# Kernel optimization log

Hardware: AMD Instinct MI355X
Metric: run time of the kernel (lower is better)

Reference implementation:

```python
import jax, jax.numpy as jnp
import numpy as np

H = 128        # num_hidden
V = 32000      # vocab_size
CD = 256       # channel_dim
T = 21         # max_seq_len (hardcoded in forward_rl)
NS = 5         # multiple_sample default
SOS, EOS = 1, 2


def setup_inputs() -> dict:
    key = jax.random.key(0)
    ks = jax.random.split(key, 12)
    s = 0.08  # param scale ~ 1/sqrt(H)
    f32 = jnp.float32
    return {
        "input_features": jax.random.normal(ks[0], (1024, CD), f32),
        "embed": (jax.random.normal(ks[1], (V, H), f32) * s),
        "W_fc": jax.random.normal(ks[2], (2 * H, CD), f32) * s,
        "b_fc": jnp.zeros((2 * H,), f32),
        "W_ih": jax.random.normal(ks[3], (4 * H, H), f32) * s,
        "b_ih": jnp.zeros((4 * H,), f32),
        "W_hh": jax.random.normal(ks[4], (4 * H, H), f32) * s,
        "b_hh": jnp.zeros((4 * H,), f32),
        "W1": jax.random.normal(ks[5], (H, H), f32) * s,
        "b1": jnp.zeros((H,), f32),
        "W2": jax.random.normal(ks[6], (V, H), f32) * s,
        "b2": jnp.zeros((V,), f32),
    }


def _decode(input_features, embed, W_fc, b_fc, W_ih, b_ih, W_hh, b_hh, W1, b1, W2, b2):
    # sample_n_times: expand each row NS times along batch
    x = jnp.repeat(input_features, NS, axis=0)           # [B, CD], B = 1024*NS
    B = x.shape[0]
    # init_hidden: from_channel_emb -> split into (h, c)
    hc = x @ W_fc.T + b_fc                               # [B, 2H]
    h0, c0 = hc[:, :H], hc[:, H:]

    it0 = jnp.full((B,), SOS, jnp.int32)
    unf0 = jnp.ones((B,), bool)

    def step(carry, _):
        h, c, it, unfinished = carry
        xt = embed[it]                                   # [B, H]
        gates = xt @ W_ih.T + b_ih + h @ W_hh.T + b_hh   # [B, 4H]
        i, f, g, o = jnp.split(gates, 4, axis=1)         # torch LSTMCell gate order
        c_new = jax.nn.sigmoid(f) * c + jax.nn.sigmoid(i) * jnp.tanh(g)
        h_new = jax.nn.sigmoid(o) * jnp.tanh(c_new)
        # classifier: Linear -> Dropout(eval: identity) -> Linear
        logits = (h_new @ W1.T + b1) @ W2.T + b2         # [B, V]
        logprobs = jax.nn.log_softmax(logits, axis=-1)
        # deterministic sampling surrogate (sample_max path): argmax
        it_new = jnp.argmax(logprobs, axis=1).astype(jnp.int32)
        sample_lp = jnp.take_along_axis(logprobs, it_new[:, None], axis=1)[:, 0]
        mask = unfinished.astype(logprobs.dtype)
        it_new = jnp.where(unfinished, it_new, 0)
        unf_new = unfinished & (it_new != EOS)
        return (h_new, c_new, it_new, unf_new), (it_new, sample_lp, mask)

    _, (seq, lps, masks) = jax.lax.scan(step, (h0, c0, it0, unf0), None, length=T)
    # scan stacks along time: [T, B] -> [B, T]
    return seq.T, lps.T, masks.T


def reference(input_features, embed, W_fc, b_fc, W_ih, b_ih, W_hh, b_hh, W1, b1, W2, b2):
    return _decode(input_features, embed, W_fc, b_fc, W_ih, b_ih, W_hh, b_hh, W1, b1, W2, b2)
```

## Files before the change

### kernel.cpp

```cpp
#include <hip/hip_runtime.h>
#include <math.h>
#include <limits.h>

#define H 128
#define V 32000
#define CD 256
#define T_STEPS 21
#define NS 5
#define SOS 1
#define EOS 2
#define B 1024
#define BFULL 5120
#define NCHUNK 250

typedef _Float16 f16;
typedef f16   half8   __attribute__((ext_vector_type(8)));
typedef float floatx4 __attribute__((ext_vector_type(4)));
typedef unsigned short ushort8v __attribute__((ext_vector_type(8)));

#define AS1 __attribute__((address_space(1)))
#define AS3 __attribute__((address_space(3)))

__device__ __forceinline__ float bf2f(unsigned short u) {
    return __uint_as_float(((unsigned)u) << 16);
}

__device__ __forceinline__ float sig32(float x) {
    float t = (float)exp(-(double)x);
    float r = __fadd_rn(1.0f, t);
    return __fdiv_rn(1.0f, r);
}
__device__ __forceinline__ float tanh32(float x) { return (float)tanh((double)x); }

__device__ __forceinline__ double w2dot(const float* __restrict__ pr,
                                        const void* __restrict__ W2_raw,
                                        int v, bool isf) {
    double acc = 0.0;
    if (isf) {
        const float* wv = (const float*)W2_raw + (long)v * H;
        #pragma unroll 8
        for (int k4 = 0; k4 < H / 4; ++k4) {
            float4 wq = *(const float4*)(wv + k4 * 4);
            float4 pq = *(const float4*)(pr + k4 * 4);
            acc += (double)pq.x * (double)wq.x;
            acc += (double)pq.y * (double)wq.y;
            acc += (double)pq.z * (double)wq.z;
            acc += (double)pq.w * (double)wq.w;
        }
    } else {
        const unsigned short* wv = (const unsigned short*)W2_raw + (long)v * H;
        #pragma unroll 8
        for (int k4 = 0; k4 < H / 4; ++k4) {
            ushort4 u = *(const ushort4*)(wv + k4 * 4);
            float4 pq = *(const float4*)(pr + k4 * 4);
            acc += (double)pq.x * (double)bf2f(u.x);
            acc += (double)pq.y * (double)bf2f(u.y);
            acc += (double)pq.z * (double)bf2f(u.z);
            acc += (double)pq.w * (double)bf2f(u.w);
        }
    }
    return acc;
}

__global__ void k_detect(const unsigned short* __restrict__ e, int* __restrict__ flag) {
    int i = threadIdx.x;
    unsigned short u = e[2 * i];
    int ex = (u >> 7) & 0xFF;
    bool wild = ((u & 0x7FFF) != 0) && (ex < 0x60 || ex > 0x8F);
    unsigned long long m = __ballot(wild);
    if (i == 0) *flag = (m != 0ull) ? 1 : 0;
}

struct TCArgs {
    const void* src[12];
    float*      dst[12];
    int         n[12];
};
__global__ __launch_bounds__(256) void k_transcode_all(TCArgs tc, const int* __restrict__ flag) {
    int which = blockIdx.y;
    float* d = tc.dst[which];
    if (d == nullptr) return;
    int i = blockIdx.x * 256 + threadIdx.x;
    if (i >= tc.n[which]) return;
    if (*flag) d[i] = ((const float*)tc.src[which])[i];
    else       d[i] = bf2f(((const unsigned short*)tc.src[which])[i]);
}

__global__ __launch_bounds__(256) void k_wtr(
    const float* __restrict__ Wih, const float* __restrict__ Whh,
    const float* __restrict__ W1, float* __restrict__ wihT,
    float* __restrict__ whhT, float* __restrict__ w1T) {
    int e = blockIdx.x * 256 + threadIdx.x;
    if (e < 512 * 128) {
        int col = e >> 7, k = e & 127;
        wihT[(k >> 1) * 1024 + col * 2 + (k & 1)] = Wih[e];
    } else if (e < 2 * 512 * 128) {
        int i = e - 512 * 128;
        int col = i >> 7, k = i & 127;
        whhT[(k >> 1) * 1024 + col * 2 + (k & 1)] = Whh[i];
    } else if (e < 2 * 512 * 128 + 128 * 128) {
        int i = e - 2 * 512 * 128;
        int col = i >> 7, k = i & 127;
        w1T[(k >> 1) * 256 + col * 2 + (k & 1)] = W1[i];
    }
}

__global__ __launch_bounds__(256) void k_wsplit(
    const void* __restrict__ W2_raw, unsigned short* __restrict__ wh,
    unsigned short* __restrict__ wl, float* __restrict__ wn,
    const int* __restrict__ flag) {
    int t = blockIdx.x * 256 + threadIdx.x;
    const bool isf = (*flag != 0);
    int vrow = t >> 4;
    int kkg  = t & 15;
    float v[8];
    if (isf) {
        float4 f0 = ((const float4*)W2_raw)[2 * t];
        float4 f1 = ((const float4*)W2_raw)[2 * t + 1];
        v[0] = f0.x; v[1] = f0.y; v[2] = f0.z; v[3] = f0.w;
        v[4] = f1.x; v[5] = f1.y; v[6] = f1.z; v[7] = f1.w;
    } else {
        ushort8v u = ((const ushort8v*)W2_raw)[t];
        #pragma unroll
        for (int i = 0; i < 8; ++i) v[i] = bf2f(u[i]);
    }
    float s = 0.f;
    half8 hv, lv;
    #pragma unroll
    for (int i = 0; i < 8; ++i) {
        s += v[i] * v[i];
        float ws = v[i] * 256.0f;
        f16 hh = (f16)ws;
        hv[i] = hh;
        lv[i] = (f16)(ws - (float)hh);
    }
    int cb = vrow >> 7, rloc = vrow & 127;
    long dst = (long)cb * 16384 + kkg * 1024 + rloc * 8;
    *(half8*)((f16*)wh + dst) = hv;
    *(half8*)((f16*)wl + dst) = lv;
    #pragma unroll
    for (int off = 1; off < 16; off <<= 1) s += __shfl_xor(s, off, 64);
    if (kkg == 0) wn[vrow] = sqrtf(s);
}

__global__ __launch_bounds__(256) void k_prep(
    const float* __restrict__ wn, float* __restrict__ wmax,
    int* __restrict__ it, int* __restrict__ unf) {
    int tid = threadIdx.x;
    if (blockIdx.x < 4) {
        int i = blockIdx.x * 256 + tid;
        it[i] = SOS; unf[i] = 1;
        return;
    }
    __shared__ float red[4];
    float m = 0.f;
    for (int i = tid; i < V; i += 256) m = fmaxf(m, wn[i]);
    #pragma unroll
    for (int off = 1; off < 64; off <<= 1) m = fmaxf(m, __shfl_xor(m, off, 64));
    if ((tid & 63) == 0) red[tid >> 6] = m;
    __syncthreads();
    if (tid == 0) *wmax = fmaxf(fmaxf(red[0], red[1]), fmaxf(red[2], red[3]));
}

__global__ __launch_bounds__(256) void k_init_hc(
    const float* __restrict__ xf, const float* __restrict__ Wfc,
    const float* __restrict__ bfc, float* __restrict__ h, float* __restrict__ c) {
    __shared__ float xl[CD];
    int r = blockIdx.x;
    int j = threadIdx.x;
    xl[j] = xf[(long)r * CD + j];
    __syncthreads();
    const float4* w4 = (const float4*)(Wfc + (long)j * CD);
    double acc = 0.0;
    for (int k4 = 0; k4 < CD / 4; ++k4) {
        float4 w = w4[k4];
        int k = k4 * 4;
        acc += (double)xl[k]     * (double)w.x;
        acc += (double)xl[k + 1] * (double)w.y;
        acc += (double)xl[k + 2] * (double)w.z;
        acc += (double)xl[k + 3] * (double)w.w;
    }
    float hc = __fadd_rn((float)acc, bfc[j]);
    if (j < H) h[(long)r * H + j] = hc;
    else       c[(long)r * H + (j - H)] = hc;
}

__global__ __launch_bounds__(512) void k_gf(
    const float* __restrict__ cmT, const float* __restrict__ csT,
    const unsigned long long* __restrict__ maskbuf,
    const void* __restrict__ W2_raw,
    const float* __restrict__ b2, const float* __restrict__ wmax,
    const void* __restrict__ embed_raw, float* __restrict__ h, float* __restrict__ c,
    const float* __restrict__ wihT, const float* __restrict__ whhT,
    const float* __restrict__ bih, const float* __restrict__ bhh,
    const float* __restrict__ w1T, const float* __restrict__ b1,
    float* __restrict__ p32, unsigned short* __restrict__ ph,
    unsigned short* __restrict__ pl, float* __restrict__ pnorm,
    int* __restrict__ it, int* __restrict__ unf, float* __restrict__ out,
    int t, const int* __restrict__ flag) {
    __shared__ float As[4][256];
    __shared__ float gsh[4][512];
    __shared__ float hl[4][132];
    __shared__ float redp[8];
    const bool isf = (*flag != 0);
    int tid = threadIdx.x;
    int rb = blockIdx.x * 4;
    int lane = tid & 63, wid = tid >> 6;

    if (t > 0 && wid < 4) {
        int r = rb + wid;
        const float* pr = p32 + (long)r * H;
        float wmx = *wmax;
        float eps = 6.0e-5f * pnorm[r] * wmx + 3e-5f;

        float marr[4];
        float AM = -__builtin_inff();
        #pragma unroll
        for (int i = 0; i < 4; ++i) {
            int cc = lane + 64 * i;
            marr[i] = (cc < NCHUNK) ? cmT[(long)cc * B + r] : -__builtin_inff();
            AM = fmaxf(AM, marr[i]);
        }
        #pragma unroll
        for (int off = 1; off < 64; off <<= 1) AM = fmaxf(AM, __shfl_xor(AM, off, 64));
        double S = 0.0;
        #pragma unroll
        for (int i = 0; i < 4; ++i) {
            int cc = lane + 64 * i;
            if (cc < NCHUNK) S += (double)csT[(long)cc * B + r];
        }
        #pragma unroll
        for (int off = 1; off < 64; off <<= 1) S += __shfl_xor(S, off, 64);

        float M = -__builtin_inff();
        #pragma unroll 1
        for (int i = 0; i < 4; ++i) {
            unsigned long long mask = __ballot(marr[i] >= AM - eps);
            while (mask) {
                int bsl = __ffsll(mask) - 1;
                mask &= mask - 1;
                int cc = i * 64 + bsl;
                const unsigned long long* mk2 = maskbuf + ((long)cc * B + r) * 2;
                #pragma unroll 1
                for (int q = 0; q < 2; ++q) {
                    if ((mk2[q] >> lane) & 1ull) {
                        int v = cc * 128 + q * 64 + lane;
                        double acc = w2dot(pr, W2_raw, v, isf);
                        float l = __fadd_rn((float)acc, b2[v]);
                        M = fmaxf(M, l);
                    }
                }
            }
        }
        #pragma unroll
        for (int off = 1; off < 64; off <<= 1) M = fmaxf(M, __shfl_xor(M, off, 64));

        float L = (float)(log(S) - (double)M);
        float negL = __fsub_rn(0.0f, L);

        int best = INT_MAX;
        #pragma unroll 1
        for (int i = 0; i < 4 && best == INT_MAX; ++i) {
            unsigned long long mask = __ballot(marr[i] >= AM - eps);
            while (mask && best == INT_MAX) {
                int bsl = __ffsll(mask) - 1;
                mask &= mask - 1;
                int cc = i * 64 + bsl;
                const unsigned long long* mk2 = maskbuf + ((long)cc * B + r) * 2;
                int hit = INT_MAX;
                #pragma unroll 1
                for (int q = 0; q < 2; ++q) {
                    if ((mk2[q] >> lane) & 1ull) {
                        int v = cc * 128 + q * 64 + lane;
                        double acc = w2dot(pr, W2_raw, v, isf);
                        float l  = __fadd_rn((float)acc, b2[v]);
                        float lp = __fsub_rn(__fsub_rn(l, M), L);
                        if (lp == negL && v < hit) hit = v;
                    }
                }
                #pragma unroll
                for (int off = 1; off < 64; off <<= 1) {
                    int oh = __shfl_xor(hit, off, 64);
                    hit = (oh < hit) ? oh : hit;
                }
                if (hit != INT_MAX) best = hit;
            }
        }
        int bi = (best == INT_MAX) ? 0 : best;

        int unfr = unf[r];
        float lp = negL;
        int itn = unfr ? bi : 0;
        int unfn = (unfr && itn != EOS) ? 1 : 0;
        if (lane == 0) { it[r] = itn; unf[r] = unfn; }
        if (lane < NS) {
            long ro = (long)r * NS + lane;
            int tm1 = t - 1;
            out[ro * T_STEPS + tm1] = (float)itn;
            out[(long)BFULL * T_STEPS + ro * T_STEPS + tm1] = lp;
            out[2L * BFULL * T_STEPS + ro * T_STEPS + tm1] = unfr ? 1.0f : 0.0f;
        }
    }
    __syncthreads();

    {
        int r = tid >> 7, kq = (tid & 127) * 2;
        long row = rb + r;
        int tok = it[row];
        float v0, v1;
        if (kq < H) {
            if (isf) {
                float2 f = *(const float2*)((const float*)embed_raw + (long)tok * H + kq);
                v0 = f.x; v1 = f.y;
            } else {
                ushort2 u = *(const ushort2*)((const unsigned short*)embed_raw + (long)tok * H + kq);
                v0 = bf2f(u.x); v1 = bf2f(u.y);
            }
        } else {
            float2 f = *(const float2*)(h + row * H + (kq - H));
            v0 = f.x; v1 = f.y;
        }
        As[r][kq] = v0; As[r][kq + 1] = v1;
    }
    __syncthreads();

    {
        int cg = tid;
        double acc[4] = {};
        const float2* wi2 = (const float2*)wihT + cg;
        #pragma unroll 8
        for (int kp = 0; kp < 64; ++kp) {
            float2 w = wi2[kp * 512];
            #pragma unroll
            for (int r = 0; r < 4; ++r) {
                float2 a2 = *(const float2*)(&As[r][kp * 2]);
                double s0 = acc[r];
                s0 += (double)a2.x * (double)w.x;
                s0 += (double)a2.y * (double)w.y;
                acc[r] = s0;
            }
        }
        float t1[4];
        float bi = bih[cg];
        #pragma unroll
        for (int r = 0; r < 4; ++r) {
            t1[r] = __fadd_rn((float)acc[r], bi);
            acc[r] = 0.0;
        }
        const float2* wh2 = (const float2*)whhT + cg;
        #pragma unroll 8
        for (int kp = 0; kp < 64; ++kp) {
            float2 w = wh2[kp * 512];
            #pragma unroll
            for (int r = 0; r < 4; ++r) {
                float2 a2 = *(const float2*)(&As[r][128 + kp * 2]);
                double s0 = acc[r];
                s0 += (double)a2.x * (double)w.x;
                s0 += (double)a2.y * (double)w.y;
                acc[r] = s0;
            }
        }
        float bh = bhh[cg];
        #pragma unroll
        for (int r = 0; r < 4; ++r)
            gsh[r][cg] = __fadd_rn(__fadd_rn(t1[r], (float)acc[r]), bh);
    }
    __syncthreads();

    {
        int lr = tid >> 7, j = tid & 127;
        long row = rb + lr;
        float gi = gsh[lr][j], gf = gsh[lr][j + 128], gg = gsh[lr][j + 256], go = gsh[lr][j + 384];
        float cv = c[row * 128 + j];
        float si = sig32(gi);
        float sf = sig32(gf);
        float so = sig32(go);
        float tg = tanh32(gg);
        float cn = __fadd_rn(__fmul_rn(sf, cv), __fmul_rn(si, tg));
        float hn = __fmul_rn(so, tanh32(cn));
        c[row * 128 + j] = cn;
        h[row * 128 + j] = hn;
        hl[lr][j] = hn;
    }
    __syncthreads();

    {
        int j = tid & 127;
        int rr = tid >> 7;
        const float2* w12 = (const float2*)w1T + j;
        double acc = 0.0;
        #pragma unroll 8
        for (int kp = 0; kp < 64; ++kp) {
            float2 w = w12[kp * 128];
            float2 a2 = *(const float2*)(&hl[rr][kp * 2]);
            acc += (double)a2.x * (double)w.x;
            acc += (double)a2.y * (double)w.y;
        }
        long row = rb + rr;
        float pv = __fadd_rn((float)acc, b1[j]);
        p32[row * H + j] = pv;
        float ps = pv * 256.0f;
        f16 hh = (f16)ps;
        f16 ll = (f16)(ps - (float)hh);
        ((f16*)ph)[row * H + j] = hh;
        ((f16*)pl)[row * H + j] = ll;
        float sq = pv * pv;
        #pragma unroll
        for (int off = 1; off < 64; off <<= 1) sq += __shfl_xor(sq, off, 64);
        if (lane == 0) redp[wid] = sq;
    }
    __syncthreads();
    if (tid < 4) pnorm[rb + tid] = sqrtf(redp[2 * tid] + redp[2 * tid + 1]);
}

__global__ __launch_bounds__(256, 2) void k_vscan_mfma(
    const unsigned short* __restrict__ ph_, const unsigned short* __restrict__ pl_,
    const unsigned short* __restrict__ whf_, const unsigned short* __restrict__ wlf_,
    const float* __restrict__ b2, const float* __restrict__ pnorm,
    const float* __restrict__ wmax,
    float* __restrict__ cmT, float* __restrict__ csT,
    unsigned long long* __restrict__ maskbuf) {
    __shared__ f16 Bsh[16384];
    __shared__ f16 Bsl[16384];
    const f16* ph  = (const f16*)ph_;
    const f16* pl  = (const f16*)pl_;
    int tid  = threadIdx.x;
    int lane = tid & 63, wid = tid >> 6;
    int tx = lane & 15, kg = lane >> 4;

    int bid = blockIdx.x;
    int xcd = bid & 7, rb = (bid >> 3) & 3, hi = bid >> 5;
    int cb = hi * 8 + xcd;
    if (cb >= NCHUNK) return;
    int rbw = rb * 256 + wid * 64;
    int vb  = cb * 128;

    {
        const f16* sh = (const f16*)whf_ + (long)cb * 16384;
        const f16* sl = (const f16*)wlf_ + (long)cb * 16384;
        #pragma unroll
        for (int i = 0; i < 8; ++i) {
            int g = tid + 256 * i;
            __builtin_amdgcn_global_load_lds(
                (const AS1 void*)(const void*)(sh + (long)g * 8),
                (AS3 void*)(void*)(Bsh + g * 8), 16, 0, 0);
            __builtin_amdgcn_global_load_lds(
                (const AS1 void*)(const void*)(sl + (long)g * 8),
                (AS3 void*)(void*)(Bsl + g * 8), 16, 0, 0);
        }
    }
    __syncthreads();

    floatx4 acc[4][8];
    #pragma unroll
    for (int m = 0; m < 4; ++m)
        #pragma unroll
        for (int n = 0; n < 8; ++n)
            acc[m][n] = (floatx4){0.f, 0.f, 0.f, 0.f};

    int aoffs[4];
    #pragma unroll
    for (int m = 0; m < 4; ++m) aoffs[m] = (rbw + m * 16 + tx) * H + kg * 8;

    #pragma unroll
    for (int kk = 0; kk < 4; ++kk) {
        half8 Ah[4], Al[4];
        #pragma unroll
        for (int m = 0; m < 4; ++m) {
            Ah[m] = *(const half8*)(ph + aoffs[m] + kk * 32);
            Al[m] = *(const half8*)(pl + aoffs[m] + kk * 32);
        }
        int bbase = (kk * 4 + kg) * 1024 + tx * 8;
        #pragma unroll
        for (int n = 0; n < 8; ++n) {
            half8 Bh = *(const half8*)(Bsh + bbase + n * 128);
            half8 Bl = *(const half8*)(Bsl + bbase + n * 128);
            #pragma unroll
            for (int m = 0; m < 4; ++m)
                acc[m][n] = __builtin_amdgcn_mfma_f32_16x16x32_f16(Ah[m], Bh, acc[m][n], 0, 0, 0);
            #pragma unroll
            for (int m = 0; m < 4; ++m)
                acc[m][n] = __builtin_amdgcn_mfma_f32_16x16x32_f16(Ah[m], Bl, acc[m][n], 0, 0, 0);
            #pragma unroll
            for (int m = 0; m < 4; ++m)
                acc[m][n] = __builtin_amdgcn_mfma_f32_16x16x32_f16(Al[m], Bh, acc[m][n], 0, 0, 0);
        }
    }

    const float S2 = 1.0f / 65536.0f;
    const float wmx = *wmax;
    float bb[8];
    #pragma unroll
    for (int n = 0; n < 8; ++n) bb[n] = b2[vb + n * 16 + tx];
    #pragma unroll
    for (int m = 0; m < 4; ++m) {
        #pragma unroll
        for (int r = 0; r < 4; ++r) {
            float l[8];
            float mxr = -__builtin_inff();
            float sr = 0.f;
            #pragma unroll
            for (int n = 0; n < 8; ++n) {
                l[n] = acc[m][n][r] * S2 + bb[n];
                mxr = fmaxf(mxr, l[n]);
                sr += __expf(l[n]);
            }
            #pragma unroll
            for (int off = 1; off < 16; off <<= 1) {
                mxr = fmaxf(mxr, __shfl_xor(mxr, off, 64));
                sr += __shfl_xor(sr, off, 64);
            }
            int row = rbw + m * 16 + kg * 4 + r;
            float thr = mxr - (6.0e-5f * pnorm[row] * wmx + 3.0e-5f);
            unsigned long long w0 = 0, w1 = 0;
            #pragma unroll
            for (int n = 0; n < 8; ++n) {
                unsigned long long bal = __ballot(l[n] >= thr);
                unsigned long long piece = (bal >> (kg * 16)) & 0xFFFFull;
                if (n < 4) w0 |= piece << (n * 16);
                else       w1 |= piece << ((n - 4) * 16);
            }
            if (tx == 0) {
                cmT[(long)cb * B + row] = mxr;
                csT[(long)cb * B + row] = sr;
                maskbuf[((long)cb * B + row) * 2]     = w0;
                maskbuf[((long)cb * B + row) * 2 + 1] = w1;
            }
        }
    }
}

__global__ __launch_bounds__(256) void k_final(
    const float* __restrict__ cmT, const float* __restrict__ csT,
    const unsigned long long* __restrict__ maskbuf,
    const float* __restrict__ p32, const void* __restrict__ W2_raw,
    const float* __restrict__ b2, const float* __restrict__ wmax,
    const float* __restrict__ pnorm,
    int* __restrict__ it, int* __restrict__ unf,
    float* __restrict__ out, int t, const int* __restrict__ flag) {
    const bool isf = (*flag != 0);
    int r = blockIdx.x * 4 + (threadIdx.x >> 6);
    int lane = threadIdx.x & 63;
    const float* pr = p32 + (long)r * H;
    float wmx = *wmax;
    float eps = 6.0e-5f * pnorm[r] * wmx + 3e-5f;

    float marr[4];
    float AM = -__builtin_inff();
    #pragma unroll
    for (int i = 0; i < 4; ++i) {
        int cc = lane + 64 * i;
        marr[i] = (cc < NCHUNK) ? cmT[(long)cc * B + r] : -__builtin_inff();
        AM = fmaxf(AM, marr[i]);
    }
    #pragma unroll
    for (int off = 1; off < 64; off <<= 1) AM = fmaxf(AM, __shfl_xor(AM, off, 64));
    double S = 0.0;
    #pragma unroll
    for (int i = 0; i < 4; ++i) {
        int cc = lane + 64 * i;
        if (cc < NCHUNK) S += (double)csT[(long)cc * B + r];
    }
    #pragma unroll
    for (int off = 1; off < 64; off <<= 1) S += __shfl_xor(S, off, 64);

    float M = -__builtin_inff();
    #pragma unroll 1
    for (int i = 0; i < 4; ++i) {
        unsigned long long mask = __ballot(marr[i] >= AM - eps);
        while (mask) {
            int b = __ffsll(mask) - 1;
            mask &= mask - 1;
            int cc = i * 64 + b;
            const unsigned long long* mk2 = maskbuf + ((long)cc * B + r) * 2;
            #pragma unroll 1
            for (int q = 0; q < 2; ++q) {
                if ((mk2[q] >> lane) & 1ull) {
                    int v = cc * 128 + q * 64 + lane;
                    double acc = w2dot(pr, W2_raw, v, isf);
                    float l = __fadd_rn((float)acc, b2[v]);
                    M = fmaxf(M, l);
                }
            }
        }
    }
    #pragma unroll
    for (int off = 1; off < 64; off <<= 1) M = fmaxf(M, __shfl_xor(M, off, 64));

    float L = (float)(log(S) - (double)M);
    float negL = __fsub_rn(0.0f, L);

    int best = INT_MAX;
    #pragma unroll 1
    for (int i = 0; i < 4 && best == INT_MAX; ++i) {
        unsigned long long mask = __ballot(marr[i] >= AM - eps);
        while (mask && best == INT_MAX) {
            int b = __ffsll(mask) - 1;
            mask &= mask - 1;
            int cc = i * 64 + b;
            const unsigned long long* mk2 = maskbuf + ((long)cc * B + r) * 2;
            int hit = INT_MAX;
            #pragma unroll 1
            for (int q = 0; q < 2; ++q) {
                if ((mk2[q] >> lane) & 1ull) {
                    int v = cc * 128 + q * 64 + lane;
                    double acc = w2dot(pr, W2_raw, v, isf);
                    float l  = __fadd_rn((float)acc, b2[v]);
                    float lp = __fsub_rn(__fsub_rn(l, M), L);
                    if (lp == negL && v < hit) hit = v;
                }
            }
            #pragma unroll
            for (int off = 1; off < 64; off <<= 1) {
                int oh = __shfl_xor(hit, off, 64);
                hit = (oh < hit) ? oh : hit;
            }
            if (hit != INT_MAX) best = hit;
        }
    }
    int bi = (best == INT_MAX) ? 0 : best;

    int unfr = unf[r];
    float lp = negL;
    int itn = unfr ? bi : 0;
    int unfn = (unfr && itn != EOS) ? 1 : 0;
    if (lane == 0) { it[r] = itn; unf[r] = unfn; }
    if (lane < NS) {
        long ro = (long)r * NS + lane;
        out[ro * T_STEPS + t] = (float)itn;
        out[(long)BFULL * T_STEPS + ro * T_STEPS + t] = lp;
        out[2L * BFULL * T_STEPS + ro * T_STEPS + t] = unfr ? 1.0f : 0.0f;
    }
}

extern "C" void kernel_launch(void* const* d_in, const int* in_sizes, int n_in,
                              void* d_out, int out_size, void* d_ws, size_t ws_size,
                              hipStream_t stream) {
    float* out = (float*)d_out;

    char* w = (char*)d_ws;
    float* fin[12];
    for (int i = 0; i < 12; ++i) {
        if (i == 1 || i == 10) { fin[i] = nullptr; continue; }
        fin[i] = (float*)w;
        size_t bytes = ((size_t)in_sizes[i] * 4 + 15) & ~(size_t)15;
        w += bytes;
    }
    float*  h     = (float*) w; w += (size_t)B * H * 4;
    float*  c     = (float*) w; w += (size_t)B * H * 4;
    float*  p32   = (float*) w; w += (size_t)B * H * 4;
    float*  cm    = (float*) w; w += (size_t)B * NCHUNK * 4;
    float*  cs    = (float*) w; w += (size_t)B * NCHUNK * 4;
    float*  wn    = (float*) w; w += (size_t)V * 4;
    float*  wmax  = (float*) w; w += 16;
    float*  pnorm = (float*) w; w += (size_t)B * 4;
    int*    it    = (int*)   w; w += (size_t)B * 4;
    int*    unf   = (int*)   w; w += (size_t)B * 4;
    int*    flag  = (int*)   w; w += 16;
    float*  wihT  = (float*) w; w += (size_t)512 * 128 * 4;
    float*  whhT  = (float*) w; w += (size_t)512 * 128 * 4;
    float*  w1T   = (float*) w; w += (size_t)128 * 128 * 4;
    unsigned long long* maskbuf = (unsigned long long*)w; w += (size_t)NCHUNK * B * 16;
    unsigned short* ph = (unsigned short*)w; w += (size_t)B * H * 2;
    unsigned short* pl = (unsigned short*)w; w += (size_t)B * H * 2;
    unsigned short* wh = (unsigned short*)w; w += (size_t)V * H * 2;
    unsigned short* wl = (unsigned short*)w; w += (size_t)V * H * 2;

    k_detect<<<1, 64, 0, stream>>>((const unsigned short*)d_in[1], flag);

    TCArgs tc;
    int maxn = 0;
    for (int i = 0; i < 12; ++i) {
        tc.src[i] = d_in[i];
        tc.dst[i] = fin[i];
        tc.n[i]   = in_sizes[i];
        if (fin[i] && in_sizes[i] > maxn) maxn = in_sizes[i];
    }
    k_transcode_all<<<dim3((maxn + 255) / 256, 12), 256, 0, stream>>>(tc, flag);

    k_wsplit<<<(V * H / 8 + 255) / 256, 256, 0, stream>>>(d_in[10], wh, wl, wn, flag);
    k_wtr<<<(2 * 512 * 128 + 128 * 128 + 255) / 256, 256, 0, stream>>>(
        fin[4], fin[6], fin[8], wihT, whhT, w1T);
    k_prep<<<5, 256, 0, stream>>>(wn, wmax, it, unf);

    const float* xf  = fin[0];
    const float* Wfc = fin[2];
    const float* bfc = fin[3];
    const float* bih = fin[5];
    const float* bhh = fin[7];
    const float* b1  = fin[9];
    const float* b2  = fin[11];

    k_init_hc<<<B, 256, 0, stream>>>(xf, Wfc, bfc, h, c);

    for (int t = 0; t < T_STEPS; ++t) {
        k_gf<<<B / 4, 512, 0, stream>>>(cm, cs, maskbuf, d_in[10], b2, wmax,
                                        d_in[1], h, c, wihT, whhT, bih, bhh,
                                        w1T, b1, p32, ph, pl, pnorm, it, unf, out, t, flag);
        k_vscan_mfma<<<1024, 256, 0, stream>>>(ph, pl, wh, wl, b2, pnorm, wmax, cm, cs, maskbuf);
    }
    k_final<<<B / 4, 256, 0, stream>>>(cm, cs, maskbuf, p32, d_in[10], b2, wmax, pnorm,
                                       it, unf, out, T_STEPS - 1, flag);
}
```

Baseline: 1.776 ms.

## Halve rows per gate block, cache candidate logits, byte-wise mask writes

k_gf now handles 2 rows per block instead of 4, launching twice as many blocks. It stages the per-chunk max and sum arrays in shared memory with coalesced float2 loads. It also keeps up to two candidate logits per lane from the max pass, so the argmax pass does not recompute the W2 dot products unless a lane has more than two candidates. k_vscan_mfma now writes the candidate mask as one byte per thread instead of ballot-packed 64-bit words, with a matching remapped bit test on the reader side. The risks are fewer rows sharing each weight load in the gate GEMV and scattered byte stores.

```diff
diff --git a/kernel.cpp b/kernel.cpp
--- a/kernel.cpp
+++ b/kernel.cpp
@@ -60,6 +60,12 @@
         }
     }
     return acc;
+}
+
+__device__ __forceinline__ bool mask_test(unsigned long long m0, unsigned long long m1, int c) {
+    int bidx = ((c & 15) << 3) + (c >> 4);
+    unsigned long long word = (bidx < 64) ? m0 : m1;
+    return (word >> (bidx & 63)) & 1ull;
 }
 
 __global__ void k_detect(const unsigned short* __restrict__ e, int* __restrict__ flag) {
@@ -198,16 +204,24 @@
     unsigned short* __restrict__ pl, float* __restrict__ pnorm,
     int* __restrict__ it, int* __restrict__ unf, float* __restrict__ out,
     int t, const int* __restrict__ flag) {
-    __shared__ float As[4][256];
-    __shared__ float gsh[4][512];
-    __shared__ float hl[4][132];
-    __shared__ float redp[8];
+    __shared__ float As[2][256];
+    __shared__ float gsh[2][512];
+    __shared__ float hl[2][132];
+    __shared__ float2 cmsh[256];
+    __shared__ float2 cssh[256];
+    __shared__ float redp[4];
     const bool isf = (*flag != 0);
     int tid = threadIdx.x;
-    int rb = blockIdx.x * 4;
+    int rb = blockIdx.x * 2;
     int lane = tid & 63, wid = tid >> 6;
 
-    if (t > 0 && wid < 4) {
+    if (t > 0 && tid < NCHUNK) {
+        cmsh[tid] = *(const float2*)(cmT + (long)tid * B + rb);
+        cssh[tid] = *(const float2*)(csT + (long)tid * B + rb);
+    }
+    __syncthreads();
+
+    if (t > 0 && wid < 2) {
         int r = rb + wid;
         const float* pr = p32 + (long)r * H;
         float wmx = *wmax;
@@ -218,7 +232,10 @@
         #pragma unroll
         for (int i = 0; i < 4; ++i) {
             int cc = lane + 64 * i;
-            marr[i] = (cc < NCHUNK) ? cmT[(long)cc * B + r] : -__builtin_inff();
+            if (cc < NCHUNK) {
+                float2 cv = cmsh[cc];
+                marr[i] = wid ? cv.y : cv.x;
+            } else marr[i] = -__builtin_inff();
             AM = fmaxf(AM, marr[i]);
         }
         #pragma unroll
@@ -227,12 +244,18 @@
         #pragma unroll
         for (int i = 0; i < 4; ++i) {
             int cc = lane + 64 * i;
-            if (cc < NCHUNK) S += (double)csT[(long)cc * B + r];
+            if (cc < NCHUNK) {
+                float2 sv = cssh[cc];
+                S += (double)(wid ? sv.y : sv.x);
+            }
         }
         #pragma unroll
         for (int off = 1; off < 64; off <<= 1) S += __shfl_xor(S, off, 64);
 
         float M = -__builtin_inff();
+        float l0f = 0.f, l1f = 0.f;
+        int v0i = 0, v1i = 0, nc = 0;
+        bool spill = false;
         #pragma unroll 1
         for (int i = 0; i < 4; ++i) {
             unsigned long long mask = __ballot(marr[i] >= AM - eps);
@@ -241,13 +264,18 @@
                 mask &= mask - 1;
                 int cc = i * 64 + bsl;
                 const unsigned long long* mk2 = maskbuf + ((long)cc * B + r) * 2;
+                unsigned long long m0 = mk2[0], m1 = mk2[1];
                 #pragma unroll 1
                 for (int q = 0; q < 2; ++q) {
-                    if ((mk2[q] >> lane) & 1ull) {
-                        int v = cc * 128 + q * 64 + lane;
+                    int cidx = q * 64 + lane;
+                    if (mask_test(m0, m1, cidx)) {
+                        int v = cc * 128 + cidx;
                         double acc = w2dot(pr, W2_raw, v, isf);
                         float l = __fadd_rn((float)acc, b2[v]);
                         M = fmaxf(M, l);
+                        if (nc == 0)      { l0f = l; v0i = v; nc = 1; }
+                        else if (nc == 1) { l1f = l; v1i = v; nc = 2; }
+                        else spill = true;
                     }
                 }
             }
@@ -259,31 +287,51 @@
         float negL = __fsub_rn(0.0f, L);
 
         int best = INT_MAX;
-        #pragma unroll 1
-        for (int i = 0; i < 4 && best == INT_MAX; ++i) {
-            unsigned long long mask = __ballot(marr[i] >= AM - eps);
-            while (mask && best == INT_MAX) {
-                int bsl = __ffsll(mask) - 1;
-                mask &= mask - 1;
-                int cc = i * 64 + bsl;
-                const unsigned long long* mk2 = maskbuf + ((long)cc * B + r) * 2;
-                int hit = INT_MAX;
-                #pragma unroll 1
-                for (int q = 0; q < 2; ++q) {
-                    if ((mk2[q] >> lane) & 1ull) {
-                        int v = cc * 128 + q * 64 + lane;
-                        double acc = w2dot(pr, W2_raw, v, isf);
-                        float l  = __fadd_rn((float)acc, b2[v]);
-                        float lp = __fsub_rn(__fsub_rn(l, M), L);
-                        if (lp == negL && v < hit) hit = v;
+        if (__ballot(spill) == 0ull) {
+            int hit = INT_MAX;
+            if (nc >= 1) {
+                float lp = __fsub_rn(__fsub_rn(l0f, M), L);
+                if (lp == negL) hit = v0i;
+            }
+            if (nc >= 2) {
+                float lp = __fsub_rn(__fsub_rn(l1f, M), L);
+                if (lp == negL && v1i < hit) hit = v1i;
+            }
+            #pragma unroll
+            for (int off = 1; off < 64; off <<= 1) {
+                int oh = __shfl_xor(hit, off, 64);
+                hit = (oh < hit) ? oh : hit;
+            }
+            best = hit;
+        } else {
+            #pragma unroll 1
+            for (int i = 0; i < 4 && best == INT_MAX; ++i) {
+                unsigned long long mask = __ballot(marr[i] >= AM - eps);
+                while (mask && best == INT_MAX) {
+                    int bsl = __ffsll(mask) - 1;
+                    mask &= mask - 1;
+                    int cc = i * 64 + bsl;
+                    const unsigned long long* mk2 = maskbuf + ((long)cc * B + r) * 2;
+                    unsigned long long m0 = mk2[0], m1 = mk2[1];
+                    int hit = INT_MAX;
+                    #pragma unroll 1
+                    for (int q = 0; q < 2; ++q) {
+                        int cidx = q * 64 + lane;
+                        if (mask_test(m0, m1, cidx)) {
+                            int v = cc * 128 + cidx;
+                            double acc = w2dot(pr, W2_raw, v, isf);
+                            float l  = __fadd_rn((float)acc, b2[v]);
+                            float lp = __fsub_rn(__fsub_rn(l, M), L);
+                            if (lp == negL && v < hit) hit = v;
+                        }
                     }
+                    #pragma unroll
+                    for (int off = 1; off < 64; off <<= 1) {
+                        int oh = __shfl_xor(hit, off, 64);
+                        hit = (oh < hit) ? oh : hit;
+                    }
+                    if (hit != INT_MAX) best = hit;
                 }
-                #pragma unroll
-                for (int off = 1; off < 64; off <<= 1) {
-                    int oh = __shfl_xor(hit, off, 64);
-                    hit = (oh < hit) ? oh : hit;
-                }
-                if (hit != INT_MAX) best = hit;
             }
         }
         int bi = (best == INT_MAX) ? 0 : best;
@@ -304,35 +352,29 @@
     __syncthreads();
 
     {
-        int r = tid >> 7, kq = (tid & 127) * 2;
+        int r = tid >> 8, kq = tid & 255;
         long row = rb + r;
         int tok = it[row];
-        float v0, v1;
+        float v0;
         if (kq < H) {
-            if (isf) {
-                float2 f = *(const float2*)((const float*)embed_raw + (long)tok * H + kq);
-                v0 = f.x; v1 = f.y;
-            } else {
-                ushort2 u = *(const ushort2*)((const unsigned short*)embed_raw + (long)tok * H + kq);
-                v0 = bf2f(u.x); v1 = bf2f(u.y);
-            }
+            if (isf) v0 = ((const float*)embed_raw)[(long)tok * H + kq];
+            else     v0 = bf2f(((const unsigned short*)embed_raw)[(long)tok * H + kq]);
         } else {
-            float2 f = *(const float2*)(h + row * H + (kq - H));
-            v0 = f.x; v1 = f.y;
-        }
-        As[r][kq] = v0; As[r][kq + 1] = v1;
+            v0 = h[row * H + (kq - H)];
+        }
+        As[r][kq] = v0;
     }
     __syncthreads();
 
     {
         int cg = tid;
-        double acc[4] = {};
+        double acc[2] = {};
         const float2* wi2 = (const float2*)wihT + cg;
         #pragma unroll 8
         for (int kp = 0; kp < 64; ++kp) {
             float2 w = wi2[kp * 512];
             #pragma unroll
-            for (int r = 0; r < 4; ++r) {
+            for (int r = 0; r < 2; ++r) {
                 float2 a2 = *(const float2*)(&As[r][kp * 2]);
                 double s0 = acc[r];
                 s0 += (double)a2.x * (double)w.x;
@@ -340,10 +382,10 @@
                 acc[r] = s0;
             }
         }
-        float t1[4];
+        float t1[2];
         float bi = bih[cg];
         #pragma unroll
-        for (int r = 0; r < 4; ++r) {
+        for (int r = 0; r < 2; ++r) {
             t1[r] = __fadd_rn((float)acc[r], bi);
             acc[r] = 0.0;
         }
@@ -352,7 +394,7 @@
         for (int kp = 0; kp < 64; ++kp) {
             float2 w = wh2[kp * 512];
             #pragma unroll
-            for (int r = 0; r < 4; ++r) {
+            for (int r = 0; r < 2; ++r) {
                 float2 a2 = *(const float2*)(&As[r][128 + kp * 2]);
                 double s0 = acc[r];
                 s0 += (double)a2.x * (double)w.x;
@@ -362,12 +404,12 @@
         }
         float bh = bhh[cg];
         #pragma unroll
-        for (int r = 0; r < 4; ++r)
+        for (int r = 0; r < 2; ++r)
             gsh[r][cg] = __fadd_rn(__fadd_rn(t1[r], (float)acc[r]), bh);
     }
     __syncthreads();
 
-    {
+    if (tid < 256) {
         int lr = tid >> 7, j = tid & 127;
         long row = rb + lr;
         float gi = gsh[lr][j], gf = gsh[lr][j + 128], gg = gsh[lr][j + 256], go = gsh[lr][j + 384];
@@ -384,7 +426,7 @@
     }
     __syncthreads();
 
-    {
+    if (tid < 256) {
         int j = tid & 127;
         int rr = tid >> 7;
         const float2* w12 = (const float2*)w1T + j;
@@ -410,7 +452,7 @@
         if (lane == 0) redp[wid] = sq;
     }
     __syncthreads();
-    if (tid < 4) pnorm[rb + tid] = sqrtf(redp[2 * tid] + redp[2 * tid + 1]);
+    if (tid < 2) pnorm[rb + tid] = sqrtf(redp[2 * tid] + redp[2 * tid + 1]);
 }
 
 __global__ __launch_bounds__(256, 2) void k_vscan_mfma(
@@ -512,19 +554,14 @@
             }
             int row = rbw + m * 16 + kg * 4 + r;
             float thr = mxr - (6.0e-5f * pnorm[row] * wmx + 3.0e-5f);
-            unsigned long long w0 = 0, w1 = 0;
-            #pragma unroll
-            for (int n = 0; n < 8; ++n) {
-                unsigned long long bal = __ballot(l[n] >= thr);
-                unsigned long long piece = (bal >> (kg * 16)) & 0xFFFFull;
-                if (n < 4) w0 |= piece << (n * 16);
-                else       w1 |= piece << ((n - 4) * 16);
-            }
+            unsigned mb = 0;
+            #pragma unroll
+            for (int n = 0; n < 8; ++n)
+                if (l[n] >= thr) mb |= (1u << n);
+            ((unsigned char*)maskbuf)[((long)cb * B + row) * 16 + tx] = (unsigned char)mb;
             if (tx == 0) {
                 cmT[(long)cb * B + row] = mxr;
                 csT[(long)cb * B + row] = sr;
-                maskbuf[((long)cb * B + row) * 2]     = w0;
-                maskbuf[((long)cb * B + row) * 2 + 1] = w1;
             }
         }
     }
@@ -573,10 +610,12 @@
             mask &= mask - 1;
             int cc = i * 64 + b;
             const unsigned long long* mk2 = maskbuf + ((long)cc * B + r) * 2;
+            unsigned long long m0 = mk2[0], m1 = mk2[1];
             #pragma unroll 1
             for (int q = 0; q < 2; ++q) {
-                if ((mk2[q] >> lane) & 1ull) {
-                    int v = cc * 128 + q * 64 + lane;
+                int cidx = q * 64 + lane;
+                if (mask_test(m0, m1, cidx)) {
+                    int v = cc * 128 + cidx;
                     double acc = w2dot(pr, W2_raw, v, isf);
                     float l = __fadd_rn((float)acc, b2[v]);
                     M = fmaxf(M, l);
@@ -599,11 +638,13 @@
             mask &= mask - 1;
             int cc = i * 64 + b;
             const unsigned long long* mk2 = maskbuf + ((long)cc * B + r) * 2;
+            unsigned long long m0 = mk2[0], m1 = mk2[1];
             int hit = INT_MAX;
             #pragma unroll 1
             for (int q = 0; q < 2; ++q) {
-                if ((mk2[q] >> lane) & 1ull) {
-                    int v = cc * 128 + q * 64 + lane;
+                int cidx = q * 64 + lane;
+                if (mask_test(m0, m1, cidx)) {
+                    int v = cc * 128 + cidx;
                     double acc = w2dot(pr, W2_raw, v, isf);
                     float l  = __fadd_rn((float)acc, b2[v]);
                     float lp = __fsub_rn(__fsub_rn(l, M), L);
@@ -694,7 +735,7 @@
     k_init_hc<<<B, 256, 0, stream>>>(xf, Wfc, bfc, h, c);
 
     for (int t = 0; t < T_STEPS; ++t) {
-        k_gf<<<B / 4, 512, 0, stream>>>(cm, cs, maskbuf, d_in[10], b2, wmax,
+        k_gf<<<B / 2, 512, 0, stream>>>(cm, cs, maskbuf, d_in[10], b2, wmax,
                                         d_in[1], h, c, wihT, whhT, bih, bhh,
                                         w1T, b1, p32, ph, pl, pnorm, it, unf, out, t, flag);
         k_vscan_mfma<<<1024, 256, 0, stream>>>(ph, pl, wh, wl, b2, pnorm, wmax, cm, cs, maskbuf);
```

Measured after the change: 1.529 ms, median of 4. 1.16x faster.
